# Kernel optimization log

Hardware: AMD Instinct MI355X
Metric: run time of the kernel (lower is better)

Reference implementation:

```python
import jax, jax.numpy as jnp
import numpy as np
import math

B, S, H, NH = 8, 2048, 256, 4
DH = H // NH
EPS = 1e-12


def setup_inputs() -> dict:
    key = jax.random.key(0)
    ks = jax.random.split(key, 20)
    g = lambda k, shape: (jax.random.normal(k, shape, jnp.float32) * 0.02)
    inp = {
        "hidden": jax.random.normal(ks[0], (B, S, H), jnp.float32),
        "Wq": g(ks[1], (H, H)), "bq": jnp.zeros((H,), jnp.float32),
        "Wk": g(ks[2], (H, H)), "bk": jnp.zeros((H,), jnp.float32),
        "Wv": g(ks[3], (H, H)), "bv": jnp.zeros((H,), jnp.float32),
        "Wo": g(ks[4], (H, H)), "bo": jnp.zeros((H,), jnp.float32),
        "W1": g(ks[5], (4 * H, H)), "b1": jnp.zeros((4 * H,), jnp.float32),
        "W2": g(ks[6], (H, 4 * H)), "b2": jnp.zeros((H,), jnp.float32),
        "ln1_w": jnp.ones((H,), jnp.float32), "ln1_b": jnp.zeros((H,), jnp.float32),
        "ln2_w": jnp.ones((H,), jnp.float32), "ln2_b": jnp.zeros((H,), jnp.float32),
        "mask": jax.random.randint(ks[7], (B, S), 0, 2, jnp.int32),
    }
    return inp


def _layernorm(x, w, b):
    u = x.mean(-1, keepdims=True)
    s = ((x - u) ** 2).mean(-1, keepdims=True)
    return w * (x - u) / jnp.sqrt(s + EPS) + b


def _gelu_tanh(h):
    return 0.5 * h * (1.0 + jnp.tanh(math.sqrt(2.0 / math.pi) * (h + 0.044715 * h ** 3)))


def _block(hidden, mask, Wq, bq, Wk, bk, Wv, bv, Wo, bo, W1, b1, W2, b2,
           ln1_w, ln1_b, ln2_w, ln2_b):
    # --- attention sublayer (pre-norm + residual) ---
    x = _layernorm(hidden, ln1_w, ln1_b)
    def heads(W, b):  # [B,S,H] -> [B,NH,S,DH]
        return (x @ W.T + b).reshape(B, S, NH, DH).transpose(0, 2, 1, 3)
    q, k, v = heads(Wq, bq), heads(Wk, bk), heads(Wv, bv)
    corr = jnp.einsum("bhqd,bhkd->bhqk", q, k) / math.sqrt(DH)
    # torch code masks QUERY rows: mask [B,S] broadcast over heads and keys
    corr = jnp.where(mask[:, None, :, None] == 0, -1e9, corr)
    prob = jax.nn.softmax(corr, axis=-1)
    attn = jnp.einsum("bhqk,bhkd->bhqd", prob, v)
    attn = attn.transpose(0, 2, 1, 3).reshape(B, S, H) @ Wo.T + bo
    hidden = hidden + attn
    # --- FFN sublayer (pre-norm + residual) ---
    y = _layernorm(hidden, ln2_w, ln2_b)
    h1 = y @ W1.T + b1
    ff = _gelu_tanh(h1) @ W2.T + b2
    return hidden + ff


def reference(hidden, Wq, bq, Wk, bk, Wv, bv, Wo, bo, W1, b1, W2, b2,
              ln1_w, ln1_b, ln2_w, ln2_b, mask):
    return _block(hidden, mask, Wq, bq, Wk, bk, Wv, bv, Wo, bo,
                  W1, b1, W2, b2, ln1_w, ln1_b, ln2_w, ln2_b)
```

## Files before the change

### kernel.cpp

```cpp
#include <hip/hip_runtime.h>
#include <hip/hip_bf16.h>
#include <cstdint>
#include <cstddef>

constexpr int CB  = 8;
constexpr int CS  = 2048;
constexpr int CH  = 256;
constexpr int CNH = 4;
constexpr int CDH = 64;
constexpr int CT  = CB * CS;

typedef __attribute__((ext_vector_type(8)))  __bf16 bf16x8;
typedef __attribute__((ext_vector_type(4)))  float  f32x4;
typedef __attribute__((ext_vector_type(16))) float  f32x16;
typedef __attribute__((ext_vector_type(2)))  int    i32x2;

__device__ __forceinline__ float b2f(unsigned short u) {
    union { float f; unsigned int i; } v; v.i = ((unsigned int)u) << 16; return v.f;
}
__device__ __forceinline__ unsigned short f2b(float f) {
    union { float f; unsigned int i; } v; v.f = f;
    unsigned int r = v.i + 0x7FFFu + ((v.i >> 16) & 1u);
    return (unsigned short)(r >> 16);
}
__device__ __forceinline__ unsigned int packbf(float a, float b) {
    float2 t; t.x = a; t.y = b;
    __hip_bfloat162 h = __float22bfloat162_rn(t);
    union { __hip_bfloat162 h; unsigned int u; } c; c.h = h; return c.u;
}
__device__ __forceinline__ float fexp2(float x) {
#if __has_builtin(__builtin_amdgcn_exp2f)
    return __builtin_amdgcn_exp2f(x);
#else
    float r; asm("v_exp_f32 %0, %1" : "=v"(r) : "v"(x)); return r;
#endif
}
__device__ __forceinline__ f32x4 mfma16(bf16x8 a, bf16x8 b, f32x4 c) {
    return __builtin_amdgcn_mfma_f32_16x16x32_bf16(a, b, c, 0, 0, 0);
}
__device__ __forceinline__ f32x16 mfma32(bf16x8 a, bf16x8 b, f32x16 c) {
    return __builtin_amdgcn_mfma_f32_32x32x16_bf16(a, b, c, 0, 0, 0);
}
__device__ __forceinline__ f32x16 zero16() {
    f32x16 z;
    #pragma unroll
    for (int i = 0; i < 16; ++i) z[i] = 0.f;
    return z;
}

#define GLOAD_LDS16(gptr, lptr)                                                        \
    __builtin_amdgcn_global_load_lds((const __attribute__((address_space(1))) void*)(gptr), \
                                     (__attribute__((address_space(3))) void*)(lptr), 16, 0, 0)

#define QSCALE 0.1803368801111204f

__global__ __launch_bounds__(256) void detect_kernel(
    const unsigned short* __restrict__ h, int* __restrict__ flag)
{
    __shared__ int s_bad;
    const int tid = threadIdx.x;
    if (tid == 0) s_bad = 0;
    __syncthreads();
    bool bad = false;
    for (int i = tid; i < 2048; i += 256) {
        float v = b2f(h[i]);
        if (!(fabsf(v) < 1e25f)) bad = true;
    }
    if (bad) s_bad = 1;
    __syncthreads();
    if (tid == 0) *flag = s_bad;
}

struct CvtW { const void* src[7]; void* dst[7]; int n[7]; };
struct CvtB { const void* src[10]; void* dst[10]; int n[10]; };

__global__ __launch_bounds__(256) void cvt_wb_k(const int* __restrict__ flag, CvtW a)
{
    const int seg = blockIdx.y, n = a.n[seg];
    const bool inf32 = (*flag != 0);
    const float* sf = (const float*)a.src[seg];
    const unsigned short* sb = (const unsigned short*)a.src[seg];
    unsigned short* d = (unsigned short*)a.dst[seg];
    for (int i = (blockIdx.x * 256 + threadIdx.x) * 4; i < n; i += gridDim.x * 1024) {
        ushort4 o;
        if (inf32) {
            float4 v = *(const float4*)(sf + i);
            o.x = f2b(v.x); o.y = f2b(v.y); o.z = f2b(v.z); o.w = f2b(v.w);
        } else {
            o = *(const ushort4*)(sb + i);
        }
        *(ushort4*)(d + i) = o;
    }
}

__global__ __launch_bounds__(256) void cvt_bf_k(const int* __restrict__ flag, CvtB a)
{
    const int seg = blockIdx.y, n = a.n[seg];
    const bool inf32 = (*flag != 0);
    const float* sf = (const float*)a.src[seg];
    const unsigned short* sb = (const unsigned short*)a.src[seg];
    float* d = (float*)a.dst[seg];
    const int i = threadIdx.x * 4;
    if (i < n) {
        float4 o;
        if (inf32) {
            o = *(const float4*)(sf + i);
        } else {
            ushort4 v = *(const ushort4*)(sb + i);
            o.x = b2f(v.x); o.y = b2f(v.y); o.z = b2f(v.z); o.w = b2f(v.w);
        }
        *(float4*)(d + i) = o;
    }
}

__global__ __launch_bounds__(256) void ln_kernel(
    const unsigned short* __restrict__ x, const float* __restrict__ w,
    const float* __restrict__ b, unsigned short* __restrict__ out)
{
    const int wave = threadIdx.x >> 6, lane = threadIdx.x & 63;
    const int token = blockIdx.x * 4 + wave;
    const int c = lane * 4;
    const size_t rowo = (size_t)token * CH + c;
    ushort4 u = *(const ushort4*)(x + rowo);
    float v0 = b2f(u.x), v1 = b2f(u.y), v2 = b2f(u.z), v3 = b2f(u.w);
    float s = v0 + v1 + v2 + v3;
    float q = v0*v0 + v1*v1 + v2*v2 + v3*v3;
    #pragma unroll
    for (int m = 1; m < 64; m <<= 1) { s += __shfl_xor(s, m, 64); q += __shfl_xor(q, m, 64); }
    float mean = s * (1.0f/256.0f);
    float var  = q * (1.0f/256.0f) - mean*mean;
    float inv  = rsqrtf(var + 1e-12f);
    float4 ww = *(const float4*)(w + c);
    float4 bb = *(const float4*)(b + c);
    ushort4 o;
    o.x = f2b(ww.x * (v0-mean)*inv + bb.x);
    o.y = f2b(ww.y * (v1-mean)*inv + bb.y);
    o.z = f2b(ww.z * (v2-mean)*inv + bb.z);
    o.w = f2b(ww.w * (v3-mean)*inv + bb.w);
    *(ushort4*)(out + rowo) = o;
}

template<bool GELU, bool RESID, bool HEADSTORE, bool OUTDYN>
__device__ __forceinline__ void gemm_core(
    const unsigned short* __restrict__ A, const unsigned short* __restrict__ W,
    const float* __restrict__ bias, const unsigned short* __restrict__ resid,
    void* __restrict__ out, const int* __restrict__ flag,
    int K, int N, int m0, int n0, float oscale)
{
    __shared__ __align__(16) unsigned short lA[128*32];
    __shared__ __align__(16) unsigned short lB[128*32];
    const int tid  = threadIdx.x;
    const int lane = tid & 63;
    const int wave = tid >> 6;
    const int wr = (wave >> 1) * 64;
    const int wc = (wave & 1) * 64;
    const int g = lane >> 4, r16 = lane & 15;
    const int lrow = lane >> 2;
    const int lch  = lane & 3;

    const f32x4 zero = {0.f, 0.f, 0.f, 0.f};
    f32x4 acc[4][4];
    #pragma unroll
    for (int m = 0; m < 4; ++m)
        #pragma unroll
        for (int n = 0; n < 4; ++n) acc[m][n] = zero;

    for (int k0 = 0; k0 < K; k0 += 32) {
        #pragma unroll
        for (int i = 0; i < 2; ++i) {
            int chunk = wave + i * 4;
            int row = chunk * 16 + lrow;
            const unsigned short* ga = A + (size_t)(m0 + row) * K + k0 + lch * 8;
            GLOAD_LDS16(ga, &lA[chunk * 512]);
            const unsigned short* gw = W + (size_t)(n0 + row) * K + k0 + lch * 8;
            GLOAD_LDS16(gw, &lB[chunk * 512]);
        }
        __syncthreads();
        bf16x8 af[4], wf[4];
        #pragma unroll
        for (int m = 0; m < 4; ++m) af[m] = *(const bf16x8*)&lA[(wr + m*16 + r16) * 32 + g * 8];
        #pragma unroll
        for (int n = 0; n < 4; ++n) wf[n] = *(const bf16x8*)&lB[(wc + n*16 + r16) * 32 + g * 8];
        #pragma unroll
        for (int m = 0; m < 4; ++m)
            #pragma unroll
            for (int n = 0; n < 4; ++n)
                acc[m][n] = mfma16(af[m], wf[n], acc[m][n]);
        __syncthreads();
    }

    const bool of32dyn = OUTDYN ? (*flag != 0) : false;
    #pragma unroll
    for (int n = 0; n < 4; ++n) {
        int col = n0 + wc + n*16 + r16;
        float bv = bias[col];
        #pragma unroll
        for (int m = 0; m < 4; ++m) {
            int row0 = m0 + wr + m*16 + g*4;
            #pragma unroll
            for (int r = 0; r < 4; ++r) {
                int row = row0 + r;
                float v = (acc[m][n][r] + bv) * oscale;
                if (GELU) {
                    float a = 0.79788456080286541f * (v + 0.044715f * v * v * v);
                    v = v * (1.0f / (1.0f + __expf(-2.0f * a)));
                }
                if (RESID) v += b2f(resid[(size_t)row * N + col]);
                size_t oidx;
                if (HEADSTORE) {
                    int hh = col >> 6, d = col & 63;
                    int bb = row >> 11, ss = row & 2047;
                    oidx = ((((size_t)bb * CNH + hh) * CS) + ss) * CDH + d;
                } else {
                    oidx = (size_t)row * N + col;
                }
                if (OUTDYN && of32dyn) ((float*)out)[oidx] = v;
                else                   ((unsigned short*)out)[oidx] = f2b(v);
            }
        }
    }
}

__global__ __launch_bounds__(256) void k_qkv(
    const unsigned short* __restrict__ xhat,
    const unsigned short* Wq, const float* bq, unsigned short* q,
    const unsigned short* Wk, const float* bk, unsigned short* k,
    const unsigned short* Wv, const float* bv, unsigned short* v)
{
    const int z  = blockIdx.x % 3;
    const int n0 = (blockIdx.x / 3) * 128;
    const int m0 = blockIdx.y * 128;
    const unsigned short* W  = z == 0 ? Wq : (z == 1 ? Wk : Wv);
    const float*          bi = z == 0 ? bq : (z == 1 ? bk : bv);
    unsigned short*       o  = z == 0 ? q  : (z == 1 ? k  : v);
    const float osc = z == 0 ? QSCALE : 1.0f;
    gemm_core<false, false, true, false>(xhat, W, bi, nullptr, o, nullptr,
                                         CH, CH, m0, n0, osc);
}

__global__ __launch_bounds__(256) void k_oproj(
    const unsigned short* __restrict__ A, const unsigned short* __restrict__ W,
    const float* __restrict__ bias, const unsigned short* __restrict__ resid,
    unsigned short* __restrict__ out)
{
    gemm_core<false, true, false, false>(A, W, bias, resid, out, nullptr,
                                         CH, CH, blockIdx.y * 128, blockIdx.x * 128, 1.0f);
}

__global__ __launch_bounds__(256) void k_ffn1(
    const unsigned short* __restrict__ A, const unsigned short* __restrict__ W,
    const float* __restrict__ bias, unsigned short* __restrict__ out)
{
    gemm_core<true, false, false, false>(A, W, bias, nullptr, out, nullptr,
                                         CH, 4*CH, blockIdx.y * 128, blockIdx.x * 128, 1.0f);
}

__global__ __launch_bounds__(256) void k_ffn2(
    const unsigned short* __restrict__ A, const unsigned short* __restrict__ W,
    const float* __restrict__ bias, const unsigned short* __restrict__ resid,
    void* __restrict__ out, const int* __restrict__ flag)
{
    gemm_core<false, true, false, true>(A, W, bias, resid, out, flag,
                                        4*CH, CH, blockIdx.y * 128, blockIdx.x * 128, 1.0f);
}

__global__ __launch_bounds__(256) void vtrans_kernel(
    const unsigned short* __restrict__ v, unsigned short* __restrict__ vt)
{
    __shared__ unsigned short T[64 * 72];
    const int bh = blockIdx.y, s0 = blockIdx.x * 64, tid = threadIdx.x;
    const size_t ibase = (size_t)bh * CS * CDH;
    const size_t obase = (size_t)bh * CDH * CS;
    #pragma unroll
    for (int i = 0; i < 2; ++i) {
        int t2 = tid + i * 256;
        int row = t2 >> 3, ch = t2 & 7;
        uint4 dv = *(const uint4*)(v + ibase + (size_t)(s0 + row) * CDH + ch * 8);
        *(uint4*)&T[row * 72 + ch * 8] = dv;
    }
    __syncthreads();
    #pragma unroll
    for (int i = 0; i < 2; ++i) {
        int t2 = tid + i * 256;
        int d = t2 >> 3, ch = t2 & 7;
        unsigned short tmp[8];
        #pragma unroll
        for (int j = 0; j < 8; ++j) tmp[j] = T[(ch * 8 + j) * 72 + d];
        *(uint4*)(vt + obase + (size_t)d * CS + s0 + ch * 8) = *(uint4*)tmp;
    }
}

__global__ __launch_bounds__(512, 4) void attn_kernel(
    const unsigned short* __restrict__ Q, const unsigned short* __restrict__ Kp,
    const unsigned short* __restrict__ Vt, const int* __restrict__ mask,
    unsigned short* __restrict__ out)
{
    __shared__ __align__(16) char lds[65536];

    const int tid = threadIdx.x, lane = tid & 63, wave = tid >> 6;
    const int qb = wave >> 1, kh = wave & 1;
    const int r32 = lane & 31, hi = lane >> 5;
    const int bh = blockIdx.y, bb = bh >> 2, hh = bh & 3;
    const int q0 = blockIdx.x * 128;
    const size_t baseQ = (size_t)bh * CS * CDH;
    const size_t baseT = (size_t)bh * CDH * CS;

    const int qrow = q0 + qb * 32 + r32;
    bf16x8 qf[4];
    {
        const bool live = (mask[bb * CS + qrow] != 0);
        #pragma unroll
        for (int dw = 0; dw < 4; ++dw) {
            uint4 v = {0u, 0u, 0u, 0u};
            if (live) v = *(const uint4*)(Q + baseQ + (size_t)qrow * CDH + dw * 16 + hi * 8);
            qf[dw] = *(bf16x8*)&v;
        }
    }

#define STAGE(BUF, KT) do {                                                             \
        _Pragma("unroll")                                                               \
        for (int i = 0; i < 2; ++i) {                                                   \
            const int slot0 = i * 512 + wave * 64;                                      \
            const int slot  = slot0 + lane;                                             \
            const int kw = slot >> 7, kk2 = slot & 127;                                 \
            GLOAD_LDS16(Kp + baseQ + (size_t)((KT) + kk2) * CDH + kw * 8,               \
                        lds + (BUF) * 16384 + slot0 * 16);                              \
            const int vc = slot >> 6, vd = slot & 63;                                   \
            GLOAD_LDS16(Vt + baseT + (size_t)vd * CS + (KT) + vc * 8,                   \
                        lds + 32768 + (BUF) * 16384 + slot0 * 16);                      \
        } } while (0)

    f32x16 o0 = zero16(), o1 = zero16();
    float psum = 0.f;

    STAGE(0, 0);
    __syncthreads();

    for (int t = 0; t < CS / 128; ++t) {
        const int buf = t & 1;
        const int kt = t * 128;
        if (t + 1 < CS / 128) STAGE(buf ^ 1, kt + 128);

        const char* kbase = lds + buf * 16384;
        const char* vbase = lds + 32768 + buf * 16384;

        f32x16 sT0 = zero16(), sT1 = zero16();
        __builtin_amdgcn_s_setprio(1);
        #pragma unroll
        for (int dw = 0; dw < 4; ++dw) {
            const char* cb = kbase + (dw * 2 + hi) * 2048;
            bf16x8 k0 = *(const bf16x8*)(cb + (kh * 64 + r32) * 16);
            bf16x8 k1 = *(const bf16x8*)(cb + (kh * 64 + 32 + r32) * 16);
            sT0 = mfma32(k0, qf[dw], sT0);
            sT1 = mfma32(k1, qf[dw], sT1);
        }
        __builtin_amdgcn_s_setprio(0);

#define PROCKB(SREG, KB) do {                                                           \
            float p[16];                                                                \
            _Pragma("unroll")                                                           \
            for (int r = 0; r < 16; ++r) { p[r] = fexp2((SREG)[r]); psum += p[r]; }     \
            _Pragma("unroll")                                                           \
            for (int w = 0; w < 2; ++w) {                                               \
                unsigned int a01 = packbf(p[w*8+0], p[w*8+1]);                          \
                unsigned int a23 = packbf(p[w*8+2], p[w*8+3]);                          \
                unsigned int b01 = packbf(p[w*8+4], p[w*8+5]);                          \
                unsigned int b23 = packbf(p[w*8+6], p[w*8+7]);                          \
                unsigned int ap0, ap1, ap2, ap3;                                        \
                {                                                                       \
                    i32x2 s1 = __builtin_amdgcn_permlane32_swap((int)a01, (int)b01, false, false); \
                    i32x2 s2 = __builtin_amdgcn_permlane32_swap((int)a23, (int)b23, false, false); \
                    ap0 = (unsigned int)s1.x; ap2 = (unsigned int)s1.y;                 \
                    ap1 = (unsigned int)s2.x; ap3 = (unsigned int)s2.y;                 \
                }                                                                       \
                union { unsigned int u[4]; bf16x8 v; } apv;                             \
                apv.u[0] = ap0; apv.u[1] = ap1; apv.u[2] = ap2; apv.u[3] = ap3;         \
                const char* vb2 = vbase + ((kh * 4 + (KB) * 2 + w) * 2 + hi) * 1024;    \
                bf16x8 v0 = *(const bf16x8*)(vb2 + r32 * 16);                           \
                bf16x8 v1 = *(const bf16x8*)(vb2 + (32 + r32) * 16);                    \
                o0 = mfma32(apv.v, v0, o0);                                             \
                o1 = mfma32(apv.v, v1, o1);                                             \
            } } while (0)

        PROCKB(sT0, 0);
        PROCKB(sT1, 1);
#undef PROCKB

        __syncthreads();
    }

    float ps = psum + __shfl_xor(psum, 32, 64);
    float* lsum = (float*)(lds + 32768);
    float* Oex  = (float*)lds;
    if (lane < 32) lsum[(qb * 2 + kh) * 32 + r32] = ps;
    if (kh == 1) {
        #pragma unroll
        for (int r = 0; r < 16; ++r) {
            const int qr = (r & 3) + 8 * (r >> 2) + 4 * hi;
            Oex[(qb * 32 + qr) * 64 + r32]      = o0[r];
            Oex[(qb * 32 + qr) * 64 + 32 + r32] = o1[r];
        }
    }
    __syncthreads();
    if (kh == 0) {
        #pragma unroll
        for (int r = 0; r < 16; ++r) {
            const int qr = (r & 3) + 8 * (r >> 2) + 4 * hi;
            const float l = lsum[(qb * 2 + 0) * 32 + qr] + lsum[(qb * 2 + 1) * 32 + qr];
            const float inv = 1.0f / l;
            const float u0 = (o0[r] + Oex[(qb * 32 + qr) * 64 + r32]) * inv;
            const float u1 = (o1[r] + Oex[(qb * 32 + qr) * 64 + 32 + r32]) * inv;
            const size_t ob = (size_t)(bb * CS + q0 + qb * 32 + qr) * CH + hh * CDH;
            out[ob + r32]      = f2b(u0);
            out[ob + 32 + r32] = f2b(u1);
        }
    }
#undef STAGE
}

extern "C" void kernel_launch(void* const* d_in, const int* in_sizes, int n_in,
                              void* d_out, int out_size, void* d_ws, size_t ws_size,
                              hipStream_t stream)
{
    const void* hidden = d_in[0];
    const void* Wq = d_in[1];  const void* bq = d_in[2];
    const void* Wk = d_in[3];  const void* bk = d_in[4];
    const void* Wv = d_in[5];  const void* bv = d_in[6];
    const void* Wo = d_in[7];  const void* bo = d_in[8];
    const void* W1 = d_in[9];  const void* b1 = d_in[10];
    const void* W2 = d_in[11]; const void* b2 = d_in[12];
    const void* ln1w = d_in[13]; const void* ln1b = d_in[14];
    const void* ln2w = d_in[15]; const void* ln2b = d_in[16];
    const int* mask = (const int*)d_in[17];

    char* ws = (char*)d_ws;
    const size_t KB = 1u << 10, MB = 1u << 20;
    int*            flag  = (int*)ws;
    float*          bqf   = (float*)(ws + 4*KB);
    float*          bkf   = (float*)(ws + 8*KB);
    float*          bvf   = (float*)(ws + 12*KB);
    float*          bof   = (float*)(ws + 16*KB);
    float*          b1f   = (float*)(ws + 20*KB);
    float*          b2f_  = (float*)(ws + 28*KB);
    float*          ln1wf = (float*)(ws + 32*KB);
    float*          ln1bf = (float*)(ws + 36*KB);
    float*          ln2wf = (float*)(ws + 40*KB);
    float*          ln2bf = (float*)(ws + 44*KB);
    unsigned short* Wqb   = (unsigned short*)(ws + 1*MB);
    unsigned short* Wkb   = (unsigned short*)(ws + 1*MB + 256*KB);
    unsigned short* Wvb   = (unsigned short*)(ws + 1*MB + 512*KB);
    unsigned short* Wob   = (unsigned short*)(ws + 1*MB + 768*KB);
    unsigned short* W1b   = (unsigned short*)(ws + 2*MB);
    unsigned short* W2b   = (unsigned short*)(ws + 2*MB + 512*KB);
    unsigned short* hb16  = (unsigned short*)(ws + 3*MB);
    unsigned short* xhat  = (unsigned short*)(ws + 11*MB);
    unsigned short* qb    = (unsigned short*)(ws + 19*MB);
    unsigned short* kb    = (unsigned short*)(ws + 27*MB);
    unsigned short* vb    = (unsigned short*)(ws + 35*MB);
    unsigned short* vtb   = (unsigned short*)(ws + 43*MB);
    unsigned short* attnb = xhat;
    unsigned short* hid2b = qb;
    unsigned short* yhat  = kb;
    unsigned short* h1g   = (unsigned short*)(ws + 51*MB);

    dim3 blk(256);
    detect_kernel<<<1, blk, 0, stream>>>((const unsigned short*)hidden, flag);

    CvtW cw;
    cw.src[0]=Wq;  cw.dst[0]=Wqb;  cw.n[0]=CH*CH;
    cw.src[1]=Wk;  cw.dst[1]=Wkb;  cw.n[1]=CH*CH;
    cw.src[2]=Wv;  cw.dst[2]=Wvb;  cw.n[2]=CH*CH;
    cw.src[3]=Wo;  cw.dst[3]=Wob;  cw.n[3]=CH*CH;
    cw.src[4]=W1;  cw.dst[4]=W1b;  cw.n[4]=4*CH*CH;
    cw.src[5]=W2;  cw.dst[5]=W2b;  cw.n[5]=4*CH*CH;
    cw.src[6]=hidden; cw.dst[6]=hb16; cw.n[6]=CT*CH;
    cvt_wb_k<<<dim3(256, 7), blk, 0, stream>>>(flag, cw);

    CvtB cf;
    cf.src[0]=bq;    cf.dst[0]=bqf;   cf.n[0]=CH;
    cf.src[1]=bk;    cf.dst[1]=bkf;   cf.n[1]=CH;
    cf.src[2]=bv;    cf.dst[2]=bvf;   cf.n[2]=CH;
    cf.src[3]=bo;    cf.dst[3]=bof;   cf.n[3]=CH;
    cf.src[4]=b1;    cf.dst[4]=b1f;   cf.n[4]=4*CH;
    cf.src[5]=b2;    cf.dst[5]=b2f_;  cf.n[5]=CH;
    cf.src[6]=ln1w;  cf.dst[6]=ln1wf; cf.n[6]=CH;
    cf.src[7]=ln1b;  cf.dst[7]=ln1bf; cf.n[7]=CH;
    cf.src[8]=ln2w;  cf.dst[8]=ln2wf; cf.n[8]=CH;
    cf.src[9]=ln2b;  cf.dst[9]=ln2bf; cf.n[9]=CH;
    cvt_bf_k<<<dim3(1, 10), blk, 0, stream>>>(flag, cf);

    ln_kernel<<<CT / 4, blk, 0, stream>>>(hb16, ln1wf, ln1bf, xhat);
    k_qkv<<<dim3(6, CT / 128), blk, 0, stream>>>(xhat, Wqb, bqf, qb,
                                                 Wkb, bkf, kb, Wvb, bvf, vb);
    vtrans_kernel<<<dim3(CS / 64, CB * CNH), blk, 0, stream>>>(vb, vtb);
    attn_kernel<<<dim3(CS / 128, CB * CNH), dim3(512), 0, stream>>>(qb, kb, vtb, mask, attnb);
    k_oproj<<<dim3(CH / 128, CT / 128), blk, 0, stream>>>(attnb, Wob, bof, hb16, hid2b);
    ln_kernel<<<CT / 4, blk, 0, stream>>>(hid2b, ln2wf, ln2bf, yhat);
    k_ffn1<<<dim3((4 * CH) / 128, CT / 128), blk, 0, stream>>>(yhat, W1b, b1f, h1g);
    k_ffn2<<<dim3(CH / 128, CT / 128), blk, 0, stream>>>(h1g, W2b, b2f_, hid2b,
                                                         d_out, flag);
}
```

Baseline: 172.1 us.

## Double-buffer GEMM LDS tiles, raise MFMA priority, reorder grid to M-major

The shared GEMM core now keeps two LDS buffers and issues the next K-tile's global-to-LDS loads before computing on the current tile, so memory latency can overlap with MFMA work. The MFMA block is wrapped in s_setprio to favour compute issue. The launch grids are also swapped so blockIdx.x walks the M dimension, and the QKV weight select moves to blockIdx.z, which changes which blocks run concurrently and how weight tiles are reused in cache. LDS use per block doubles, which may lower occupancy.

```diff
diff --git a/kernel.cpp b/kernel.cpp
--- a/kernel.cpp
+++ b/kernel.cpp
@@ -147,8 +147,8 @@
     void* __restrict__ out, const int* __restrict__ flag,
     int K, int N, int m0, int n0, float oscale)
 {
-    __shared__ __align__(16) unsigned short lA[128*32];
-    __shared__ __align__(16) unsigned short lB[128*32];
+    __shared__ __align__(16) unsigned short lA[2][128*32];
+    __shared__ __align__(16) unsigned short lB[2][128*32];
     const int tid  = threadIdx.x;
     const int lane = tid & 63;
     const int wave = tid >> 6;
@@ -158,6 +158,17 @@
     const int lrow = lane >> 2;
     const int lch  = lane & 3;
 
+#define GSTAGE(BUF, K0) do {                                                            \
+        _Pragma("unroll")                                                               \
+        for (int i = 0; i < 2; ++i) {                                                   \
+            int chunk = wave + i * 4;                \
+            int row = chunk * 16 + lrow;                                                \
+            const unsigned short* ga = A + (size_t)(m0 + row) * K + (K0) + lch * 8;     \
+            GLOAD_LDS16(ga, &lA[BUF][chunk * 512]);                                     \
+            const unsigned short* gw = W + (size_t)(n0 + row) * K + (K0) + lch * 8;     \
+            GLOAD_LDS16(gw, &lB[BUF][chunk * 512]);                                     \
+        } } while (0)
+
     const f32x4 zero = {0.f, 0.f, 0.f, 0.f};
     f32x4 acc[4][4];
     #pragma unroll
@@ -165,29 +176,27 @@
         #pragma unroll
         for (int n = 0; n < 4; ++n) acc[m][n] = zero;
 
-    for (int k0 = 0; k0 < K; k0 += 32) {
-        #pragma unroll
-        for (int i = 0; i < 2; ++i) {
-            int chunk = wave + i * 4;
-            int row = chunk * 16 + lrow;
-            const unsigned short* ga = A + (size_t)(m0 + row) * K + k0 + lch * 8;
-            GLOAD_LDS16(ga, &lA[chunk * 512]);
-            const unsigned short* gw = W + (size_t)(n0 + row) * K + k0 + lch * 8;
-            GLOAD_LDS16(gw, &lB[chunk * 512]);
-        }
-        __syncthreads();
+    GSTAGE(0, 0);
+    __syncthreads();
+    const int NT = K >> 5;
+    for (int t = 0; t < NT; ++t) {
+        const int cur = t & 1;
+        if (t + 1 < NT) GSTAGE(cur ^ 1, (t + 1) * 32);
         bf16x8 af[4], wf[4];
         #pragma unroll
-        for (int m = 0; m < 4; ++m) af[m] = *(const bf16x8*)&lA[(wr + m*16 + r16) * 32 + g * 8];
-        #pragma unroll
-        for (int n = 0; n < 4; ++n) wf[n] = *(const bf16x8*)&lB[(wc + n*16 + r16) * 32 + g * 8];
+        for (int m = 0; m < 4; ++m) af[m] = *(const bf16x8*)&lA[cur][(wr + m*16 + r16) * 32 + g * 8];
+        #pragma unroll
+        for (int n = 0; n < 4; ++n) wf[n] = *(const bf16x8*)&lB[cur][(wc + n*16 + r16) * 32 + g * 8];
+        __builtin_amdgcn_s_setprio(1);
         #pragma unroll
         for (int m = 0; m < 4; ++m)
             #pragma unroll
             for (int n = 0; n < 4; ++n)
                 acc[m][n] = mfma16(af[m], wf[n], acc[m][n]);
+        __builtin_amdgcn_s_setprio(0);
         __syncthreads();
     }
+#undef GSTAGE
 
     const bool of32dyn = OUTDYN ? (*flag != 0) : false;
     #pragma unroll
@@ -227,15 +236,12 @@
     const unsigned short* Wk, const float* bk, unsigned short* k,
     const unsigned short* Wv, const float* bv, unsigned short* v)
 {
-    const int z  = blockIdx.x % 3;
-    const int n0 = (blockIdx.x / 3) * 128;
-    const int m0 = blockIdx.y * 128;
-    const unsigned short* W  = z == 0 ? Wq : (z == 1 ? Wk : Wv);
-    const float*          bi = z == 0 ? bq : (z == 1 ? bk : bv);
-    unsigned short*       o  = z == 0 ? q  : (z == 1 ? k  : v);
-    const float osc = z == 0 ? QSCALE : 1.0f;
+    const unsigned short* W  = blockIdx.z == 0 ? Wq : (blockIdx.z == 1 ? Wk : Wv);
+    const float*          bi = blockIdx.z == 0 ? bq : (blockIdx.z == 1 ? bk : bv);
+    unsigned short*       o  = blockIdx.z == 0 ? q  : (blockIdx.z == 1 ? k  : v);
+    const float osc = blockIdx.z == 0 ? QSCALE : 1.0f;
     gemm_core<false, false, true, false>(xhat, W, bi, nullptr, o, nullptr,
-                                         CH, CH, m0, n0, osc);
+                                         CH, CH, blockIdx.x * 128, blockIdx.y * 128, osc);
 }
 
 __global__ __launch_bounds__(256) void k_oproj(
@@ -244,7 +250,7 @@
     unsigned short* __restrict__ out)
 {
     gemm_core<false, true, false, false>(A, W, bias, resid, out, nullptr,
-                                         CH, CH, blockIdx.y * 128, blockIdx.x * 128, 1.0f);
+                                         CH, CH, blockIdx.x * 128, blockIdx.y * 128, 1.0f);
 }
 
 __global__ __launch_bounds__(256) void k_ffn1(
@@ -252,7 +258,7 @@
     const float* __restrict__ bias, unsigned short* __restrict__ out)
 {
     gemm_core<true, false, false, false>(A, W, bias, nullptr, out, nullptr,
-                                         CH, 4*CH, blockIdx.y * 128, blockIdx.x * 128, 1.0f);
+                                         CH, 4*CH, blockIdx.x * 128, blockIdx.y * 128, 1.0f);
 }
 
 __global__ __launch_bounds__(256) void k_ffn2(
@@ -261,7 +267,7 @@
     void* __restrict__ out, const int* __restrict__ flag)
 {
     gemm_core<false, true, false, true>(A, W, bias, resid, out, flag,
-                                        4*CH, CH, blockIdx.y * 128, blockIdx.x * 128, 1.0f);
+                                        4*CH, CH, blockIdx.x * 128, blockIdx.y * 128, 1.0f);
 }
 
 __global__ __launch_bounds__(256) void vtrans_kernel(
@@ -490,13 +496,13 @@
     cvt_bf_k<<<dim3(1, 10), blk, 0, stream>>>(flag, cf);
 
     ln_kernel<<<CT / 4, blk, 0, stream>>>(hb16, ln1wf, ln1bf, xhat);
-    k_qkv<<<dim3(6, CT / 128), blk, 0, stream>>>(xhat, Wqb, bqf, qb,
-                                                 Wkb, bkf, kb, Wvb, bvf, vb);
+    k_qkv<<<dim3(CT / 128, CH / 128, 3), blk, 0, stream>>>(xhat, Wqb, bqf, qb,
+                                                           Wkb, bkf, kb, Wvb, bvf, vb);
     vtrans_kernel<<<dim3(CS / 64, CB * CNH), blk, 0, stream>>>(vb, vtb);
     attn_kernel<<<dim3(CS / 128, CB * CNH), dim3(512), 0, stream>>>(qb, kb, vtb, mask, attnb);
-    k_oproj<<<dim3(CH / 128, CT / 128), blk, 0, stream>>>(attnb, Wob, bof, hb16, hid2b);
+    k_oproj<<<dim3(CT / 128, CH / 128), blk, 0, stream>>>(attnb, Wob, bof, hb16, hid2b);
     ln_kernel<<<CT / 4, blk, 0, stream>>>(hid2b, ln2wf, ln2bf, yhat);
-    k_ffn1<<<dim3((4 * CH) / 128, CT / 128), blk, 0, stream>>>(yhat, W1b, b1f, h1g);
-    k_ffn2<<<dim3(CH / 128, CT / 128), blk, 0, stream>>>(h1g, W2b, b2f_, hid2b,
+    k_ffn1<<<dim3(CT / 128, (4 * CH) / 128), blk, 0, stream>>>(yhat, W1b, b1f, h1g);
+    k_ffn2<<<dim3(CT / 128, CH / 128), blk, 0, stream>>>(h1g, W2b, b2f_, hid2b,
                                                          d_out, flag);
 }
```

Result: no change. 172.1 us (+0.0%).

## Template GEMM tile sizes, use BK=64 with k-major LDS layout, smaller tiles

Applied to the files above, without the earlier changes.

The shared GEMM core is templated on tile dimensions. Each main-loop iteration now loads a 64-wide K slab through a k-major LDS slot layout and issues two MFMA sub-steps per barrier pair. The QKV, FFN1, O-proj and FFN2 kernels switch to 64x128 or 64x64 tiles. The grids are reordered so the M dimension is on blockIdx.x, and QKV uses blockIdx.z to select the weight. The aim is more blocks for occupancy on small-N GEMMs, fewer barriers per K step, and better L2 locality; the cost is less operand reuse per tile.

```diff
diff --git a/kernel.cpp b/kernel.cpp
--- a/kernel.cpp
+++ b/kernel.cpp
@@ -140,62 +140,78 @@
     *(ushort4*)(out + rowo) = o;
 }
 
-template<bool GELU, bool RESID, bool HEADSTORE, bool OUTDYN>
+template<int MT, int NT, bool GELU, bool RESID, bool HEADSTORE, bool OUTDYN>
 __device__ __forceinline__ void gemm_core(
     const unsigned short* __restrict__ A, const unsigned short* __restrict__ W,
     const float* __restrict__ bias, const unsigned short* __restrict__ resid,
     void* __restrict__ out, const int* __restrict__ flag,
     int K, int N, int m0, int n0, float oscale)
 {
-    __shared__ __align__(16) unsigned short lA[128*32];
-    __shared__ __align__(16) unsigned short lB[128*32];
+    constexpr int ASLOT = 8 * MT;
+    constexpr int WSLOT = 8 * NT;
+    constexpr int NGRP  = (ASLOT + WSLOT) / 64;
+    constexpr int FM = MT / 32, FN = NT / 32;
+    __shared__ __align__(16) unsigned short lA[ASLOT * 8];
+    __shared__ __align__(16) unsigned short lB[WSLOT * 8];
+
     const int tid  = threadIdx.x;
     const int lane = tid & 63;
     const int wave = tid >> 6;
-    const int wr = (wave >> 1) * 64;
-    const int wc = (wave & 1) * 64;
+    const int wr = (wave >> 1) * (MT / 2);
+    const int wc = (wave & 1) * (NT / 2);
     const int g = lane >> 4, r16 = lane & 15;
-    const int lrow = lane >> 2;
-    const int lch  = lane & 3;
 
     const f32x4 zero = {0.f, 0.f, 0.f, 0.f};
-    f32x4 acc[4][4];
+    f32x4 acc[FM][FN];
     #pragma unroll
-    for (int m = 0; m < 4; ++m)
-        #pragma unroll
-        for (int n = 0; n < 4; ++n) acc[m][n] = zero;
-
-    for (int k0 = 0; k0 < K; k0 += 32) {
-        #pragma unroll
-        for (int i = 0; i < 2; ++i) {
-            int chunk = wave + i * 4;
-            int row = chunk * 16 + lrow;
-            const unsigned short* ga = A + (size_t)(m0 + row) * K + k0 + lch * 8;
-            GLOAD_LDS16(ga, &lA[chunk * 512]);
-            const unsigned short* gw = W + (size_t)(n0 + row) * K + k0 + lch * 8;
-            GLOAD_LDS16(gw, &lB[chunk * 512]);
+    for (int m = 0; m < FM; ++m)
+        #pragma unroll
+        for (int n = 0; n < FN; ++n) acc[m][n] = zero;
+
+    for (int k0 = 0; k0 < K; k0 += 64) {
+        #pragma unroll
+        for (int j = 0; j < NGRP / 4; ++j) {
+            const int gi = j * 4 + wave;
+            const int s0 = gi * 64;
+            const int s  = s0 + lane;
+            if (s0 < ASLOT) {
+                const int kw = s / MT, row = s % MT;
+                GLOAD_LDS16(A + (size_t)(m0 + row) * K + k0 + kw * 8,
+                            (char*)lA + s0 * 16);
+            } else {
+                const int s2 = s - ASLOT;
+                const int kw = s2 / NT, row = s2 % NT;
+                GLOAD_LDS16(W + (size_t)(n0 + row) * K + k0 + kw * 8,
+                            (char*)lB + (s0 - ASLOT) * 16);
+            }
         }
         __syncthreads();
-        bf16x8 af[4], wf[4];
-        #pragma unroll
-        for (int m = 0; m < 4; ++m) af[m] = *(const bf16x8*)&lA[(wr + m*16 + r16) * 32 + g * 8];
-        #pragma unroll
-        for (int n = 0; n < 4; ++n) wf[n] = *(const bf16x8*)&lB[(wc + n*16 + r16) * 32 + g * 8];
-        #pragma unroll
-        for (int m = 0; m < 4; ++m)
+        #pragma unroll
+        for (int kk = 0; kk < 2; ++kk) {
+            bf16x8 af[FM], wf[FN];
+            const int kwb = kk * 4 + g;
             #pragma unroll
-            for (int n = 0; n < 4; ++n)
-                acc[m][n] = mfma16(af[m], wf[n], acc[m][n]);
+            for (int m = 0; m < FM; ++m)
+                af[m] = *(const bf16x8*)&lA[(kwb * MT + wr + m*16 + r16) * 8];
+            #pragma unroll
+            for (int n = 0; n < FN; ++n)
+                wf[n] = *(const bf16x8*)&lB[(kwb * NT + wc + n*16 + r16) * 8];
+            #pragma unroll
+            for (int m = 0; m < FM; ++m)
+                #pragma unroll
+                for (int n = 0; n < FN; ++n)
+                    acc[m][n] = mfma16(af[m], wf[n], acc[m][n]);
+        }
         __syncthreads();
     }
 
     const bool of32dyn = OUTDYN ? (*flag != 0) : false;
     #pragma unroll
-    for (int n = 0; n < 4; ++n) {
+    for (int n = 0; n < FN; ++n) {
         int col = n0 + wc + n*16 + r16;
         float bv = bias[col];
         #pragma unroll
-        for (int m = 0; m < 4; ++m) {
+        for (int m = 0; m < FM; ++m) {
             int row0 = m0 + wr + m*16 + g*4;
             #pragma unroll
             for (int r = 0; r < 4; ++r) {
@@ -227,15 +243,12 @@
     const unsigned short* Wk, const float* bk, unsigned short* k,
     const unsigned short* Wv, const float* bv, unsigned short* v)
 {
-    const int z  = blockIdx.x % 3;
-    const int n0 = (blockIdx.x / 3) * 128;
-    const int m0 = blockIdx.y * 128;
-    const unsigned short* W  = z == 0 ? Wq : (z == 1 ? Wk : Wv);
-    const float*          bi = z == 0 ? bq : (z == 1 ? bk : bv);
-    unsigned short*       o  = z == 0 ? q  : (z == 1 ? k  : v);
-    const float osc = z == 0 ? QSCALE : 1.0f;
-    gemm_core<false, false, true, false>(xhat, W, bi, nullptr, o, nullptr,
-                                         CH, CH, m0, n0, osc);
+    const unsigned short* W  = blockIdx.z == 0 ? Wq : (blockIdx.z == 1 ? Wk : Wv);
+    const float*          bi = blockIdx.z == 0 ? bq : (blockIdx.z == 1 ? bk : bv);
+    unsigned short*       o  = blockIdx.z == 0 ? q  : (blockIdx.z == 1 ? k  : v);
+    const float osc = blockIdx.z == 0 ? QSCALE : 1.0f;
+    gemm_core<64, 128, false, false, true, false>(xhat, W, bi, nullptr, o, nullptr,
+                                                  CH, CH, blockIdx.x * 64, blockIdx.y * 128, osc);
 }
 
 __global__ __launch_bounds__(256) void k_oproj(
@@ -243,16 +256,16 @@
     const float* __restrict__ bias, const unsigned short* __restrict__ resid,
     unsigned short* __restrict__ out)
 {
-    gemm_core<false, true, false, false>(A, W, bias, resid, out, nullptr,
-                                         CH, CH, blockIdx.y * 128, blockIdx.x * 128, 1.0f);
+    gemm_core<64, 64, false, true, false, false>(A, W, bias, resid, out, nullptr,
+                                                 CH, CH, blockIdx.x * 64, blockIdx.y * 64, 1.0f);
 }
 
 __global__ __launch_bounds__(256) void k_ffn1(
     const unsigned short* __restrict__ A, const unsigned short* __restrict__ W,
     const float* __restrict__ bias, unsigned short* __restrict__ out)
 {
-    gemm_core<true, false, false, false>(A, W, bias, nullptr, out, nullptr,
-                                         CH, 4*CH, blockIdx.y * 128, blockIdx.x * 128, 1.0f);
+    gemm_core<64, 128, true, false, false, false>(A, W, bias, nullptr, out, nullptr,
+                                                  CH, 4*CH, blockIdx.x * 64, blockIdx.y * 128, 1.0f);
 }
 
 __global__ __launch_bounds__(256) void k_ffn2(
@@ -260,8 +273,8 @@
     const float* __restrict__ bias, const unsigned short* __restrict__ resid,
     void* __restrict__ out, const int* __restrict__ flag)
 {
-    gemm_core<false, true, false, true>(A, W, bias, resid, out, flag,
-                                        4*CH, CH, blockIdx.y * 128, blockIdx.x * 128, 1.0f);
+    gemm_core<64, 64, false, true, false, true>(A, W, bias, resid, out, flag,
+                                                4*CH, CH, blockIdx.x * 64, blockIdx.y * 64, 1.0f);
 }
 
 __global__ __launch_bounds__(256) void vtrans_kernel(
@@ -490,13 +503,13 @@
     cvt_bf_k<<<dim3(1, 10), blk, 0, stream>>>(flag, cf);
 
     ln_kernel<<<CT / 4, blk, 0, stream>>>(hb16, ln1wf, ln1bf, xhat);
-    k_qkv<<<dim3(6, CT / 128), blk, 0, stream>>>(xhat, Wqb, bqf, qb,
-                                                 Wkb, bkf, kb, Wvb, bvf, vb);
+    k_qkv<<<dim3(CT / 64, CH / 128, 3), blk, 0, stream>>>(xhat, Wqb, bqf, qb,
+                                                          Wkb, bkf, kb, Wvb, bvf, vb);
     vtrans_kernel<<<dim3(CS / 64, CB * CNH), blk, 0, stream>>>(vb, vtb);
     attn_kernel<<<dim3(CS / 128, CB * CNH), dim3(512), 0, stream>>>(qb, kb, vtb, mask, attnb);
-    k_oproj<<<dim3(CH / 128, CT / 128), blk, 0, stream>>>(attnb, Wob, bof, hb16, hid2b);
+    k_oproj<<<dim3(CT / 64, CH / 64), blk, 0, stream>>>(attnb, Wob, bof, hb16, hid2b);
     ln_kernel<<<CT / 4, blk, 0, stream>>>(hid2b, ln2wf, ln2bf, yhat);
-    k_ffn1<<<dim3((4 * CH) / 128, CT / 128), blk, 0, stream>>>(yhat, W1b, b1f, h1g);
-    k_ffn2<<<dim3(CH / 128, CT / 128), blk, 0, stream>>>(h1g, W2b, b2f_, hid2b,
-                                                         d_out, flag);
-}
+    k_ffn1<<<dim3(CT / 64, (4 * CH) / 128), blk, 0, stream>>>(yhat, W1b, b1f, h1g);
+    k_ffn2<<<dim3(CT / 64, CH / 64), blk, 0, stream>>>(h1g, W2b, b2f_, hid2b,
+                                                       d_out, flag);
+}
```

Measured after the change: 191.5 us. 11.3% more time.
